# Kernel optimization log

Hardware: AMD Instinct MI355X
Metric: run time of the kernel (lower is better)

The kernel has to match this reference:

```python
import jax, jax.numpy as jnp
import numpy as np

NEG = -1e9
EPS = 1e-5


def _layernorm(x, g, b):
    m = x.mean(-1, keepdims=True)
    v = ((x - m) ** 2).mean(-1, keepdims=True)
    return (x - m) / jnp.sqrt(v + EPS) * g + b


def _layer(h_aug, H_inc, mask_neg, W1, W1_hat, ctx1, W2, W2_hat, W3, g, b):
    # h_aug: (T, H), H_inc/mask_neg: (T, E)
    H = h_aug.shape[-1]
    scale = 1.0 / jnp.sqrt(jnp.asarray(H, h_aug.dtype))
    # Stage 1: node -> hyperedge attention
    proj_hat = h_aug @ W1_hat.T                       # (T, H)
    raw = (proj_hat * ctx1).sum(-1) * scale           # (T,)
    score = raw[:, None] + mask_neg                   # (T, E)
    alpha = jax.nn.softmax(score, axis=0) * H_inc     # (T, E)
    hyper = alpha.T @ (h_aug @ W1.T)                  # (E, H)
    # Stage 2: hyperedge -> node attention
    proj2_hat = hyper @ W2_hat.T                      # (E, H)
    score_ne = (h_aug @ W3.T) @ proj2_hat.T * scale + mask_neg  # (T, E)
    beta = jax.nn.softmax(score_ne, axis=1) * H_inc   # (T, E)
    out = beta @ (hyper @ W2.T)                       # (T, H)
    return _layernorm(out + h_aug, g, b)


def reference(node_emb, H_inc, membership, W1, W1_hat, ctx1, W2, W2_hat, W3, ln_g, ln_b, region_init):
    B, N, H = node_emb.shape
    R = region_init.shape[0]
    L = W1.shape[0]
    mask_neg = jnp.where(H_inc == 0, NEG, 0.0).astype(node_emb.dtype)
    counts = jax.ops.segment_sum(jnp.ones((N,), node_emb.dtype), membership, num_segments=R)
    safe_counts = jnp.maximum(counts, 1.0)

    def per_sample(h):  # h: (N, H)
        sums = jax.ops.segment_sum(h, membership, num_segments=R)     # (R, H)
        reg = jnp.where(counts[:, None] > 0, sums / safe_counts[:, None], 0.0)
        reg = reg + region_init
        h_aug = jnp.concatenate([h, reg], axis=0)                     # (N+R, H)
        for l in range(L):
            h_aug = _layer(h_aug, H_inc, mask_neg, W1[l], W1_hat[l], ctx1[l],
                           W2[l], W2_hat[l], W3[l], ln_g[l], ln_b[l])
        return h_aug[:N]

    return jax.vmap(per_sample)(node_emb)


def setup_inputs() -> dict:
    key = jax.random.key(0)
    ks = jax.random.split(key, 12)
    B, N, R, E, H, L = 4, 8000, 16, 1024, 128, 2
    T = N + R
    w_std = 1.0 / np.sqrt(H)
    node_emb = jax.random.normal(ks[0], (B, N, H), dtype=jnp.float32)
    H_inc = (jax.random.uniform(ks[1], (T, E)) < 0.05).astype(jnp.float32)
    membership = jax.random.randint(ks[2], (N,), 0, R, dtype=jnp.int32)
    W1 = jax.random.normal(ks[3], (L, H, H), dtype=jnp.float32) * w_std
    W1_hat = jax.random.normal(ks[4], (L, H, H), dtype=jnp.float32) * w_std
    ctx1 = jax.random.normal(ks[5], (L, H), dtype=jnp.float32) * 0.02
    W2 = jax.random.normal(ks[6], (L, H, H), dtype=jnp.float32) * w_std
    W2_hat = jax.random.normal(ks[7], (L, H, H), dtype=jnp.float32) * w_std
    W3 = jax.random.normal(ks[8], (L, H, H), dtype=jnp.float32) * w_std
    ln_g = jnp.ones((L, H), dtype=jnp.float32)
    ln_b = jnp.zeros((L, H), dtype=jnp.float32)
    region_init = jax.random.normal(ks[9], (R, H), dtype=jnp.float32) * 0.02
    return {"node_emb": node_emb, "H_inc": H_inc, "membership": membership,
            "W1": W1, "W1_hat": W1_hat, "ctx1": ctx1, "W2": W2, "W2_hat": W2_hat,
            "W3": W3, "ln_g": ln_g, "ln_b": ln_b, "region_init": region_init}
```

## Files before the change

kernel.cpp:

```cpp
#include <hip/hip_runtime.h>

#define HD 128
#define CAPE 768
#define MAXR 16
#define NB_RS 128
#define RF_CH 16
#define KSTR 136
#define VSTR 72

typedef unsigned short u16;
typedef unsigned long long u64;
typedef __attribute__((ext_vector_type(8))) short bf16x8;
typedef __attribute__((ext_vector_type(4))) float f32x4;
typedef __attribute__((ext_vector_type(4))) unsigned u32x4;

__device__ inline float b2f(unsigned u){ return __uint_as_float(u << 16); }
__device__ inline float b2fhi(unsigned u){ return __uint_as_float(u & 0xffff0000u); }
__device__ inline u16 f2b(float x){
  unsigned u = __float_as_uint(x);
  return (u16)((u + 0x7fffu + ((u >> 16) & 1u)) >> 16);
}

__device__ inline float waveSum(float v){ for(int o=32;o;o>>=1) v += __shfl_down(v,o); return v; }
__device__ inline float waveMax(float v){ for(int o=32;o;o>>=1) v = fmaxf(v,__shfl_down(v,o)); return v; }

__device__ inline float blockSum128(float v, float* red){
  int j = threadIdx.x;
  float s = waveSum(v);
  __syncthreads();
  if ((j & 63) == 0) red[j >> 6] = s;
  __syncthreads();
  return red[0] + red[1];
}
__device__ inline float blockMax128(float v, float* red){
  int j = threadIdx.x;
  float s = waveMax(v);
  __syncthreads();
  if ((j & 63) == 0) red[j >> 6] = s;
  __syncthreads();
  return fmaxf(red[0], red[1]);
}

__global__ void k_count(const int* __restrict__ memb, int N, int* __restrict__ counts){
  __shared__ int h[64];
  int tid = threadIdx.x;
  if (tid < 64) h[tid] = 0;
  __syncthreads();
  for (int t = blockIdx.x*blockDim.x + tid; t < N; t += gridDim.x*blockDim.x)
    atomicAdd(&h[memb[t]], 1);
  __syncthreads();
  if (tid < 64){ int v = h[tid]; if (v) atomicAdd(&counts[tid], v); }
}

__global__ __launch_bounds__(128) void k_regsum_fast(const float* __restrict__ node,
                        const int* __restrict__ memb, int N, int R,
                        float* __restrict__ partials){
  int b = blockIdx.y, j = threadIdx.x, blk = blockIdx.x;
  int nb = gridDim.x;
  int per = (N + nb - 1) / nb;
  int t0 = blk * per;
  int t1 = t0 + per; if (t1 > N) t1 = N;
  float acc[MAXR];
  #pragma unroll
  for (int i = 0; i < MAXR; ++i) acc[i] = 0.f;
  const float* base = node + (long)b*N*HD + j;
  #pragma unroll 4
  for (int t = t0; t < t1; ++t){
    float v = base[(long)t*HD];
    int r = memb[t];
    #pragma unroll
    for (int i = 0; i < MAXR; ++i) acc[i] += (i == r) ? v : 0.f;
  }
  float* dst = partials + ((long)(b*nb + blk)*R)*HD + j;
  #pragma unroll
  for (int i = 0; i < MAXR; ++i)
    if (i < R) dst[(long)i*HD] = acc[i];
}

__global__ void k_regsum_lds(const float* __restrict__ node, const int* __restrict__ memb,
                             int N, int R, float* __restrict__ partials, int nb){
  extern __shared__ float acc[];
  int b = blockIdx.y, j = threadIdx.x;
  for (int r = 0; r < R; ++r) acc[r*HD + j] = 0.f;
  int per = (N + gridDim.x - 1) / gridDim.x;
  int t0 = blockIdx.x * per;
  int t1 = t0 + per; if (t1 > N) t1 = N;
  for (int t = t0; t < t1; ++t){
    int r = memb[t];
    acc[r*HD + j] += node[((long)b*N + t)*HD + j];
  }
  for (int r = 0; r < R; ++r)
    atomicAdd(&partials[((long)(b*nb)*R + r)*HD + j], acc[r*HD + j]);
}

__global__ __launch_bounds__(128) void k_regfin1b(const float* __restrict__ partials,
                         int nb, int redN, int R, int total, float* __restrict__ red2){
  int c = blockIdx.y;
  int i = blockIdx.x*128 + threadIdx.x;
  if (i >= total) return;
  int j = i % HD;
  int r = (i / HD) % R;
  int b = i / (HD * R);
  int per = (redN + RF_CH - 1) / RF_CH;
  int k0 = c*per, k1 = k0 + per; if (k1 > redN) k1 = redN;
  float s = 0.f;
  for (int blk = k0; blk < k1; ++blk)
    s += partials[((long)(b*nb + blk)*R + r)*HD + j];
  red2[(long)c*total + i] = s;
}

__global__ void k_regfin2(const float* __restrict__ red2, int total,
                          const int* __restrict__ counts,
                          const float* __restrict__ rinit, float* __restrict__ h_aug,
                          int N, int R, int T, int B){
  int i = blockIdx.x*blockDim.x + threadIdx.x;
  if (i >= total) return;
  int j = i % HD; int r = (i/HD) % R; int b = i/(HD*R);
  float s = 0.f;
  #pragma unroll
  for (int c = 0; c < RF_CH; ++c)
    s += red2[(long)c*total + i];
  int cnt = counts[r];
  float v = (cnt > 0) ? s / (float)cnt : 0.f;
  v += rinit[r*HD + j];
  h_aug[((long)b*T + N + r)*HD + j] = v;
}

__global__ __launch_bounds__(128) void k_copyraw(const float* __restrict__ node,
                      const float* __restrict__ v, float* __restrict__ h_aug,
                      float* __restrict__ raw, int N, int T, float scale){
  int t = blockIdx.x, b = blockIdx.y, j = threadIdx.x;
  __shared__ float red[2];
  long rowb = (long)b*T + t;
  float x;
  if (t < N){ x = node[((long)b*N + t)*HD + j]; h_aug[rowb*HD + j] = x; }
  else      { x = h_aug[rowb*HD + j]; }
  float s = blockSum128(x * v[j], red);
  if (j == 0) raw[rowb] = s * scale;
}

__global__ __launch_bounds__(256) void k_maskbuild(const float* __restrict__ Hinc, int E, int MW,
                        u64* __restrict__ maskw){
  int t = blockIdx.x;
  int wv = threadIdx.x >> 6, lane = threadIdx.x & 63;
  const float* hrow = Hinc + (long)t*E;
  for (int w = wv; w < MW; w += 4){
    int e = w*64 + lane;
    bool f = (e < E) && (hrow[e] != 0.f);
    u64 mk = __ballot(f);
    if (lane == 0) maskw[(long)t*MW + w] = mk;
  }
}

__global__ __launch_bounds__(256) void k_colbuild2(const u64* __restrict__ maskw, int T, int MW,
                           u16* __restrict__ colidx, int* __restrict__ colcnt){
  int e = blockIdx.x;
  int w = e >> 6, bit = e & 63;
  int j = threadIdx.x;
  int lane = j & 63, wv = j >> 6;
  __shared__ int wsum[4];
  int c = 0;
  for (int base = 0; base < T; base += 256){
    int t = base + j;
    bool f = (t < T) && ((maskw[(long)t*MW + w] >> bit) & 1ull);
    u64 mk = __ballot(f);
    if (lane == 0) wsum[wv] = __popcll(mk);
    __syncthreads();
    int pre = 0;
    #pragma unroll
    for (int k = 0; k < 4; ++k) pre += (k < wv) ? wsum[k] : 0;
    int tot = wsum[0] + wsum[1] + wsum[2] + wsum[3];
    if (f){
      int pos = c + pre + (int)__popcll(mk & ((1ull << lane) - 1ull));
      if (pos < CAPE) colidx[(long)e*CAPE + pos] = (u16)t;
    }
    c += tot;
    __syncthreads();
  }
  if (j == 0) colcnt[e] = (c < CAPE) ? c : CAPE;
}

__global__ void k_ctxv(const float* __restrict__ ctx1, const float* __restrict__ W1h,
                       float* __restrict__ v){
  int l = blockIdx.x, k = threadIdx.x;
  float a = 0.f;
  for (int j = 0; j < HD; ++j) a += ctx1[l*HD + j] * W1h[((long)l*HD + j)*HD + k];
  v[l*HD + k] = a;
}

__global__ void k_mm128(const float* __restrict__ W2h, const float* __restrict__ W3,
                        float* __restrict__ MqT){
  int n = blockIdx.x, l = blockIdx.y, k = threadIdx.x;
  const float* A = W2h + (long)l*HD*HD;
  const float* Bm = W3 + (long)l*HD*HD;
  float s = 0.f;
  for (int j = 0; j < HD; ++j) s += A[(long)j*HD + n] * Bm[(long)j*HD + k];
  MqT[((long)l*HD + n)*HD + k] = s;
}

__global__ __launch_bounds__(256) void k_gemmM(const float* __restrict__ A,
                       const float* __restrict__ Wa, const float* __restrict__ Wb,
                       u16* __restrict__ Ca, u16* __restrict__ Cb, int M){
  const float* W = blockIdx.y ? Wb : Wa;
  u16* C = blockIdx.y ? Cb : Ca;
  __shared__ __align__(16) u16 Ws[128][KSTR];
  __shared__ __align__(16) u16 As[64][KSTR];
  int tid = threadIdx.x;
  int row0 = blockIdx.x * 64;
  for (int i = tid; i < 128*128; i += 256){
    int r = i >> 7, c = i & 127;
    Ws[r][c] = f2b(W[(long)r*HD + c]);
  }
  for (int i = tid; i < 64*128; i += 256){
    int r = i >> 7, c = i & 127;
    int gr = row0 + r;
    As[r][c] = (gr < M) ? f2b(A[(long)gr*HD + c]) : (u16)0;
  }
  __syncthreads();

  int wave = tid >> 6, lane = tid & 63;
  int wr0 = wave * 16;
  int frow = lane & 15;
  int koff = (lane >> 4) * 8;
  f32x4 acc[8];
  #pragma unroll
  for (int f = 0; f < 8; ++f) acc[f] = (f32x4){0.f,0.f,0.f,0.f};

  #pragma unroll
  for (int ks = 0; ks < 4; ++ks){
    int kc = ks*32 + koff;
    bf16x8 av = *(const bf16x8*)&As[wr0 + frow][kc];
    #pragma unroll
    for (int f = 0; f < 8; ++f){
      bf16x8 bv = *(const bf16x8*)&Ws[f*16 + frow][kc];
      acc[f] = __builtin_amdgcn_mfma_f32_16x16x32_bf16(av, bv, acc[f], 0, 0, 0);
    }
  }

  int orow = wr0 + (lane >> 4) * 4;
  #pragma unroll
  for (int f = 0; f < 8; ++f){
    int col = f*16 + frow;
    #pragma unroll
    for (int i = 0; i < 4; ++i){
      int gr = row0 + orow + i;
      if (gr < M) C[(long)gr*HD + col] = f2b(acc[f][i]);
    }
  }
}

__global__ __launch_bounds__(256) void k_gemmW2T(const float* __restrict__ W2,
                       const u16* __restrict__ hyb, u16* __restrict__ hw2t, int E){
  int b = blockIdx.y;
  int e0 = blockIdx.x * 64;
  __shared__ __align__(16) u16 As[128][KSTR];
  __shared__ __align__(16) u16 Bs[64][KSTR];
  int tid = threadIdx.x;
  for (int i = tid; i < 128*128; i += 256){
    int r = i >> 7, c = i & 127;
    As[r][c] = f2b(W2[(long)r*HD + c]);
  }
  {
    int er = tid >> 2, q = (tid & 3)*32;
    if (e0 + er < E){
      const uint4* src = (const uint4*)(hyb + ((long)b*E + e0 + er)*HD + q);
      uint4 w0 = src[0], w1 = src[1], w2 = src[2], w3 = src[3];
      *(uint4*)&Bs[er][q]    = w0;
      *(uint4*)&Bs[er][q+8]  = w1;
      *(uint4*)&Bs[er][q+16] = w2;
      *(uint4*)&Bs[er][q+24] = w3;
    } else {
      uint4 z = {0,0,0,0};
      *(uint4*)&Bs[er][q] = z; *(uint4*)&Bs[er][q+8] = z;
      *(uint4*)&Bs[er][q+16] = z; *(uint4*)&Bs[er][q+24] = z;
    }
  }
  __syncthreads();
  int wv = tid >> 6, lane = tid & 63;
  int lc = lane & 15, lg = lane >> 4;
  f32x4 acc[2][4];
  #pragma unroll
  for (int mt=0;mt<2;++mt)
    #pragma unroll
    for (int nf=0;nf<4;++nf) acc[mt][nf] = (f32x4){0.f,0.f,0.f,0.f};
  #pragma unroll
  for (int mt=0;mt<2;++mt){
    int hr = wv*32 + mt*16 + lc;
    #pragma unroll
    for (int ks=0;ks<4;++ks){
      bf16x8 av = *(const bf16x8*)&As[hr][ks*32 + lg*8];
      #pragma unroll
      for (int nf=0;nf<4;++nf){
        bf16x8 bv = *(const bf16x8*)&Bs[nf*16+lc][ks*32 + lg*8];
        acc[mt][nf] = __builtin_amdgcn_mfma_f32_16x16x32_bf16(av, bv, acc[mt][nf], 0,0,0);
      }
    }
  }
  #pragma unroll
  for (int mt=0;mt<2;++mt){
    #pragma unroll
    for (int nf=0;nf<4;++nf){
      #pragma unroll
      for (int i=0;i<4;++i){
        int h = wv*32 + mt*16 + lg*4 + i;
        int e = e0 + nf*16 + lc;
        if (e < E) hw2t[((long)b*HD + h)*E + e] = f2b(acc[mt][nf][i]);
      }
    }
  }
}

__global__ __launch_bounds__(128) void k_edge(int swz, const float* __restrict__ raw,
                      const u16* __restrict__ proj1b,
                      const int* __restrict__ colcnt, const u16* __restrict__ colidx,
                      u16* __restrict__ hyb, int T, int E){
  int bi = blockIdx.x;
  int b, e;
  if (swz){ int x = bi & 7; b = x >> 1; e = ((bi >> 3) << 1) | (x & 1); }
  else    { b = bi / E; e = bi - b*E; }
  int j = threadIdx.x;
  int lane = j & 63, w = j >> 6;
  __shared__ float red[2];
  __shared__ float wls[CAPE];
  __shared__ int   tls[CAPE];
  __shared__ float part[128];
  int c = colcnt[e]; if (c > CAPE) c = CAPE;
  const u16* ci = colidx + (long)e*CAPE;
  const float* rawb = raw + (long)b*T;
  unsigned* orow = (unsigned*)(hyb + ((long)b*E + e)*HD);
  if (c <= 0){ if (w == 0) orow[lane] = 0u; return; }
  float lm = -1e30f;
  for (int i = j; i < c; i += 128){
    int t = ci[i];
    float v = rawb[t];
    tls[i] = t;
    wls[i] = v;
    lm = fmaxf(lm, v);
  }
  float m = blockMax128(lm, red);
  float lz = 0.f;
  for (int i = j; i < c; i += 128){
    float x = __expf(wls[i] - m);
    wls[i] = x;
    lz += x;
  }
  float Z = blockSum128(lz, red);
  float invZ = 1.f / Z;
  const u16* pb = proj1b + (long)b*T*HD + 2*lane;
  float a00=0.f,a01=0.f,a10=0.f,a11=0.f;
  int i = w;
  for (; i + 2 < c; i += 4){
    int t0v = tls[i], t1v = tls[i+2];
    float w0 = wls[i], w1 = wls[i+2];
    unsigned u0 = *(const unsigned*)(pb + (long)t0v*HD);
    unsigned u1 = *(const unsigned*)(pb + (long)t1v*HD);
    a00 += w0 * b2f(u0 & 0xffffu);  a01 += w0 * b2fhi(u0);
    a10 += w1 * b2f(u1 & 0xffffu);  a11 += w1 * b2fhi(u1);
  }
  for (; i < c; i += 2){
    float w0 = wls[i];
    unsigned u0 = *(const unsigned*)(pb + (long)tls[i]*HD);
    a00 += w0 * b2f(u0 & 0xffffu);  a01 += w0 * b2fhi(u0);
  }
  float o0 = a00 + a10, o1 = a01 + a11;
  __syncthreads();
  if (w == 1){ part[lane*2] = o0; part[lane*2+1] = o1; }
  __syncthreads();
  if (w == 0){
    o0 = (o0 + part[lane*2])   * invZ;
    o1 = (o1 + part[lane*2+1]) * invZ;
    orow[lane] = (unsigned)f2b(o0) | ((unsigned)f2b(o1) << 16);
  }
}

__global__ __launch_bounds__(256) void k_flashp(
      const u16* __restrict__ qtb, const u16* __restrict__ hyb, const u16* __restrict__ hw2t,
      const u64* __restrict__ maskw,
      u16* __restrict__ Opart, float* __restrict__ mpart, float* __restrict__ lpart,
      int T, int E, int half, float scale){
  int b = blockIdx.y, Bc = gridDim.y;
  int s = blockIdx.z, nsplit = gridDim.z;
  int t0 = blockIdx.x * 64;
  int tid = threadIdx.x;
  int wv = tid >> 6, lane = tid & 63;
  int lc = lane & 15, lg = lane >> 4;

  __shared__ __align__(16) u16 Ks[64][KSTR];
  __shared__ __align__(16) u16 Vs[128][VSTR];

  int MW = (E + 63) >> 6;
  int ntile = (E + 63) / 64;
  int et0 = s * half;
  int etend = (s == nsplit-1) ? ntile : ((s+1)*half < ntile ? (s+1)*half : ntile);

  int qrow = t0 + wv*16 + lc;
  bf16x8 qf[4];
  if (qrow < T){
    const u16* qr = qtb + ((long)b*T + qrow)*HD + lg*8;
    #pragma unroll
    for (int ks = 0; ks < 4; ++ks) qf[ks] = *(const bf16x8*)(qr + ks*32);
  } else {
    #pragma unroll
    for (int ks = 0; ks < 4; ++ks) qf[ks] = (bf16x8){0,0,0,0,0,0,0,0};
  }

  float m_s = -1e30f, l_s = 0.f;
  f32x4 Oa[8];
  #pragma unroll
  for (int f=0;f<8;++f) Oa[f] = (f32x4){0.f,0.f,0.f,0.f};

  const u16* hyB = hyb + (long)b*E*HD;
  const u16* vtB = hw2t + (long)b*HD*E;

  int kr = tid >> 2, kq = (tid & 3)*32;
  int vh = tid >> 1, vo = (tid & 1)*32;

  uint4 kreg0, kreg1, kreg2, kreg3, vreg0, vreg1, vreg2, vreg3;
  const uint4 zz = make_uint4(0u,0u,0u,0u);

  if (et0 < etend){
    int e0 = et0*64;
    if (e0 + kr < E){
      const uint4* sp = (const uint4*)(hyB + (long)(e0+kr)*HD + kq);
      kreg0=sp[0]; kreg1=sp[1]; kreg2=sp[2]; kreg3=sp[3];
    } else { kreg0=zz; kreg1=zz; kreg2=zz; kreg3=zz; }
    if (e0 + vo + 31 < E){
      const uint4* sp = (const uint4*)(vtB + (long)vh*E + e0 + vo);
      vreg0=sp[0]; vreg1=sp[1]; vreg2=sp[2]; vreg3=sp[3];
    } else {
      union { uint4 v[4]; u16 s[32]; } u;
      #pragma unroll
      for (int k=0;k<32;++k){ int e=e0+vo+k; u.s[k] = (e<E)? vtB[(long)vh*E+e] : (u16)0; }
      vreg0=u.v[0]; vreg1=u.v[1]; vreg2=u.v[2]; vreg3=u.v[3];
    }
  }

  for (int et = et0; et < etend; ++et){
    *(uint4*)&Ks[kr][kq]    = kreg0;
    *(uint4*)&Ks[kr][kq+8]  = kreg1;
    *(uint4*)&Ks[kr][kq+16] = kreg2;
    *(uint4*)&Ks[kr][kq+24] = kreg3;
    {
      int eb0 = vo;        int ne0 = eb0>>4; int ka0 = (ne0>>1)*32 + ((eb0>>2)&3)*8 + (ne0&1)*4;
      int eb1 = vo + 8;    int ne1 = eb1>>4; int ka1 = (ne1>>1)*32 + ((eb1>>2)&3)*8 + (ne1&1)*4;
      int eb2 = vo + 16;   int ne2 = eb2>>4; int ka2 = (ne2>>1)*32 + ((eb2>>2)&3)*8 + (ne2&1)*4;
      int eb3 = vo + 24;   int ne3 = eb3>>4; int ka3 = (ne3>>1)*32 + ((eb3>>2)&3)*8 + (ne3&1)*4;
      *(uint2*)&Vs[vh][ka0]   = make_uint2(vreg0.x, vreg0.y);
      *(uint2*)&Vs[vh][ka0+8] = make_uint2(vreg0.z, vreg0.w);
      *(uint2*)&Vs[vh][ka1]   = make_uint2(vreg1.x, vreg1.y);
      *(uint2*)&Vs[vh][ka1+8] = make_uint2(vreg1.z, vreg1.w);
      *(uint2*)&Vs[vh][ka2]   = make_uint2(vreg2.x, vreg2.y);
      *(uint2*)&Vs[vh][ka2+8] = make_uint2(vreg2.z, vreg2.w);
      *(uint2*)&Vs[vh][ka3]   = make_uint2(vreg3.x, vreg3.y);
      *(uint2*)&Vs[vh][ka3+8] = make_uint2(vreg3.z, vreg3.w);
    }
    __syncthreads();
    if (et + 1 < etend){
      int e0 = (et+1)*64;
      if (e0 + kr < E){
        const uint4* sp = (const uint4*)(hyB + (long)(e0+kr)*HD + kq);
        kreg0=sp[0]; kreg1=sp[1]; kreg2=sp[2]; kreg3=sp[3];
      } else { kreg0=zz; kreg1=zz; kreg2=zz; kreg3=zz; }
      if (e0 + vo + 31 < E){
        const uint4* sp = (const uint4*)(vtB + (long)vh*E + e0 + vo);
        vreg0=sp[0]; vreg1=sp[1]; vreg2=sp[2]; vreg3=sp[3];
      } else {
        union { uint4 v[4]; u16 s[32]; } u;
        #pragma unroll
        for (int k=0;k<32;++k){ int e=e0+vo+k; u.s[k] = (e<E)? vtB[(long)vh*E+e] : (u16)0; }
        vreg0=u.v[0]; vreg1=u.v[1]; vreg2=u.v[2]; vreg3=u.v[3];
      }
    }

    u64 mw = (qrow < T) ? maskw[(long)qrow*MW + et] : 0ull;

    f32x4 accS[4];
    #pragma unroll
    for (int ne=0;ne<4;++ne) accS[ne] = (f32x4){0.f,0.f,0.f,0.f};
    __builtin_amdgcn_s_setprio(1);
    #pragma unroll
    for (int ks=0;ks<4;++ks){
      #pragma unroll
      for (int ne=0;ne<4;++ne){
        bf16x8 kv = *(const bf16x8*)&Ks[ne*16+lc][ks*32 + lg*8];
        accS[ne] = __builtin_amdgcn_mfma_f32_16x16x32_bf16(kv, qf[ks], accS[ne], 0,0,0);
      }
    }
    __builtin_amdgcn_s_setprio(0);

    unsigned lo = (unsigned)mw, hi = (unsigned)(mw >> 32);
    unsigned nib[4];
    nib[0] = (lo >> (lg*4)) & 0xFu;
    nib[1] = (lo >> (16 + lg*4)) & 0xFu;
    nib[2] = (hi >> (lg*4)) & 0xFu;
    nib[3] = (hi >> (16 + lg*4)) & 0xFu;

    float p[4][4];
    float mx = -3e30f;
    #pragma unroll
    for (int ne=0;ne<4;++ne){
      #pragma unroll
      for (int r=0;r<4;++r){
        float sv = ((nib[ne] >> r) & 1u) ? accS[ne][r]*scale : -3e30f;
        p[ne][r] = sv;
        mx = fmaxf(mx, sv);
      }
    }
    mx = fmaxf(mx, __shfl_xor(mx, 16));
    mx = fmaxf(mx, __shfl_xor(mx, 32));

    float corr = 1.f;
    if (!__all(mx <= m_s + 8.f)){
      float mn = fmaxf(m_s, mx);
      corr = __expf(m_s - mn);
      m_s = mn;
      float corrO[4];
      #pragma unroll
      for (int i=0;i<4;++i) corrO[i] = __shfl(corr, lg*4 + i, 16);
      #pragma unroll
      for (int f=0;f<8;++f){
        #pragma unroll
        for (int i=0;i<4;++i) Oa[f][i] *= corrO[i];
      }
    }

    float ls = 0.f;
    #pragma unroll
    for (int ne=0;ne<4;++ne){
      #pragma unroll
      for (int r=0;r<4;++r){
        float pv = __expf(p[ne][r] - m_s);
        p[ne][r] = pv;
        ls += pv;
      }
    }
    ls += __shfl_xor(ls, 16);
    ls += __shfl_xor(ls, 32);
    l_s = l_s*corr + ls;

    unsigned pk00, pk01, pk10, pk11, pk20, pk21, pk30, pk31;
    asm("v_cvt_pk_bf16_f32 %0, %1, %2" : "=v"(pk00) : "v"(p[0][0]), "v"(p[0][1]));
    asm("v_cvt_pk_bf16_f32 %0, %1, %2" : "=v"(pk01) : "v"(p[0][2]), "v"(p[0][3]));
    asm("v_cvt_pk_bf16_f32 %0, %1, %2" : "=v"(pk10) : "v"(p[1][0]), "v"(p[1][1]));
    asm("v_cvt_pk_bf16_f32 %0, %1, %2" : "=v"(pk11) : "v"(p[1][2]), "v"(p[1][3]));
    asm("v_cvt_pk_bf16_f32 %0, %1, %2" : "=v"(pk20) : "v"(p[2][0]), "v"(p[2][1]));
    asm("v_cvt_pk_bf16_f32 %0, %1, %2" : "=v"(pk21) : "v"(p[2][2]), "v"(p[2][3]));
    asm("v_cvt_pk_bf16_f32 %0, %1, %2" : "=v"(pk30) : "v"(p[3][0]), "v"(p[3][1]));
    asm("v_cvt_pk_bf16_f32 %0, %1, %2" : "=v"(pk31) : "v"(p[3][2]), "v"(p[3][3]));

    __builtin_amdgcn_s_setprio(1);
    {
      u32x4 w0v = { pk00, pk01, pk10, pk11 };
      bf16x8 pa0 = __builtin_bit_cast(bf16x8, w0v);
      #pragma unroll
      for (int f=0;f<8;++f){
        bf16x8 vb = *(const bf16x8*)&Vs[f*16+lc][lg*8];
        Oa[f] = __builtin_amdgcn_mfma_f32_16x16x32_bf16(pa0, vb, Oa[f], 0,0,0);
      }
      u32x4 w1v = { pk20, pk21, pk30, pk31 };
      bf16x8 pa1 = __builtin_bit_cast(bf16x8, w1v);
      #pragma unroll
      for (int f=0;f<8;++f){
        bf16x8 vb = *(const bf16x8*)&Vs[f*16+lc][32 + lg*8];
        Oa[f] = __builtin_amdgcn_mfma_f32_16x16x32_bf16(pa1, vb, Oa[f], 0,0,0);
      }
    }
    __builtin_amdgcn_s_setprio(0);
    __syncthreads();
  }

  u16* Ob = Opart + (((long)s*Bc + b)*T)*HD;
  #pragma unroll
  for (int i=0;i<4;++i){
    int t = t0 + wv*16 + lg*4 + i;
    if (t >= T) continue;
    #pragma unroll
    for (int f=0;f<8;++f)
      Ob[(long)t*HD + f*16 + lc] = f2b(Oa[f][i]);
  }
  if (lg == 0 && qrow < T){
    long mlrow = ((long)s*Bc + b)*T + qrow;
    mpart[mlrow] = m_s;
    lpart[mlrow] = l_s;
  }
}

__global__ __launch_bounds__(128) void k_merge(
      const u16* __restrict__ Opart, const float* __restrict__ mpart, const float* __restrict__ lpart,
      int nsplit,
      const float* __restrict__ lng, const float* __restrict__ lnb,
      const float* __restrict__ vnext, float* __restrict__ rawnext, int writeRaw,
      float* __restrict__ h_aug, float* __restrict__ out,
      int T, int N, int writeOut, float scale){
  int t = blockIdx.x, b = blockIdx.y, j = threadIdx.x;
  int Bc = gridDim.y;
  __shared__ float red[2];
  long r0 = ((long)b)*T + t;
  long r1 = ((long)Bc + b)*T + t;
  float m0 = mpart[r0], l0 = lpart[r0];
  float m1 = (nsplit > 1) ? mpart[r1] : -1e30f;
  float l1 = (nsplit > 1) ? lpart[r1] : 0.f;
  float M = fmaxf(m0, m1);
  float c0 = __expf(m0 - M), c1 = __expf(m1 - M);
  float l = l0*c0 + l1*c1;
  float inv = (l > 0.f) ? 1.f/l : 0.f;
  float o = b2f(Opart[r0*HD + j]) * c0;
  if (nsplit > 1) o += b2f(Opart[r1*HD + j]) * c1;
  o *= inv;
  long rowb = (long)b*T + t;
  float x = o + h_aug[rowb*HD + j];
  float mean = blockSum128(x, red) * (1.f/HD);
  float d = x - mean;
  float var = blockSum128(d*d, red) * (1.f/HD);
  float y = d * rsqrtf(var + 1e-5f) * lng[j] + lnb[j];
  if (writeOut){
    if (t < N) out[((long)b*N + t)*HD + j] = y;
  } else {
    h_aug[rowb*HD + j] = y;
  }
  if (writeRaw){
    float s = blockSum128(y * vnext[j], red);
    if (j == 0) rawnext[rowb] = s * scale;
  }
}

extern "C" void kernel_launch(void* const* d_in, const int* in_sizes, int n_in,
                              void* d_out, int out_size, void* d_ws, size_t ws_size,
                              hipStream_t stream) {
  const float* node_emb = (const float*)d_in[0];
  const float* Hinc     = (const float*)d_in[1];
  const int*   memb     = (const int*)d_in[2];
  const float* W1       = (const float*)d_in[3];
  const float* W1h      = (const float*)d_in[4];
  const float* ctx1     = (const float*)d_in[5];
  const float* W2       = (const float*)d_in[6];
  const float* W2h      = (const float*)d_in[7];
  const float* W3       = (const float*)d_in[8];
  const float* lng      = (const float*)d_in[9];
  const float* lnb      = (const float*)d_in[10];
  const float* rinit    = (const float*)d_in[11];
  float* out = (float*)d_out;

  const int N  = in_sizes[2];
  const int Hd = in_sizes[3] / in_sizes[5];
  const int L  = in_sizes[5] / Hd;
  const int R  = in_sizes[11] / Hd;
  const int B  = in_sizes[0] / (N * Hd);
  const int T  = N + R;
  const int E  = in_sizes[1] / T;
  const int MW = (E + 63) / 64;
  const float scale = 1.0f / sqrtf((float)Hd);

  char* p = (char*)d_ws;
  auto carve = [&](size_t bytes){ char* r = p; p += (bytes + 255) & ~(size_t)255; return (void*)r; };
  float* h_aug  = (float*)carve((size_t)B*T*Hd*4);
  u16*   proj1b = (u16*)  carve((size_t)B*T*Hd*2);
  u16*   qtb    = (u16*)  carve((size_t)B*T*Hd*2);
  u16*   hyb    = (u16*)  carve((size_t)B*E*Hd*2);
  u16*   hw2t   = (u16*)  carve((size_t)B*Hd*E*2);
  float* MqT    = (float*)carve((size_t)L*Hd*Hd*4);
  float* rawb   = (float*)carve((size_t)B*T*4);
  float* vbuf   = (float*)carve((size_t)L*Hd*4);
  u64*   maskw  = (u64*)  carve((size_t)T*MW*8);
  int* counts   = (int*)carve((size_t)R*4);
  int* col_cnt  = (int*)carve((size_t)E*4);
  u16* col_idx  = (u16*)carve((size_t)E*CAPE*2);
  float* mpart  = (float*)carve((size_t)2*B*T*4);
  float* lpart  = (float*)carve((size_t)2*B*T*4);
  float* red2   = (float*)carve((size_t)RF_CH*B*MAXR*Hd*4);

  size_t used = (size_t)(p - (char*)d_ws);
  size_t rem  = (ws_size > used) ? (ws_size - used) : 0;
  size_t needP  = (size_t)B*NB_RS*R*Hd*4;
  size_t needO2 = (size_t)2*B*T*Hd*2;
  size_t need2 = needP > needO2 ? needP : needO2;
  int SPLIT = (rem >= need2) ? 2 : 1;
  float* partials = (float*)p;
  u16*   Opart    = (u16*)p;

  hipMemsetAsync(counts, 0, (size_t)R*4, stream);

  k_count<<<32, 256, 0, stream>>>(memb, N, counts);

  int total = B*R*Hd;
  int redN;
  if (R <= MAXR){
    k_regsum_fast<<<dim3(NB_RS, B), 128, 0, stream>>>(node_emb, memb, N, R, partials);
    redN = NB_RS;
  } else {
    hipMemsetAsync(partials, 0, (size_t)B*R*Hd*4, stream);
    k_regsum_lds<<<dim3(16, B), Hd, (size_t)R*Hd*4, stream>>>(node_emb, memb, N, R, partials, NB_RS);
    redN = 1;
  }
  k_regfin1b<<<dim3((total+127)/128, RF_CH), 128, 0, stream>>>(partials, NB_RS, redN, R, total, red2);
  k_regfin2<<<(total+255)/256, 256, 0, stream>>>(red2, total, counts, rinit, h_aug, N, R, T, B);

  k_maskbuild<<<T, 256, 0, stream>>>(Hinc, E, MW, maskw);
  k_colbuild2<<<E, 256, 0, stream>>>(maskw, T, MW, col_idx, col_cnt);

  k_ctxv<<<L, Hd, 0, stream>>>(ctx1, W1h, vbuf);
  k_mm128<<<dim3(Hd, L), Hd, 0, stream>>>(W2h, W3, MqT);
  k_copyraw<<<dim3(T, B), 128, 0, stream>>>(node_emb, vbuf, h_aug, rawb, N, T, scale);

  int MT = B*T;
  int gTm = (MT + 63)/64;
  int gTf = (T + 63)/64;
  int gEt = (E + 63)/64;
  int ntile = (E + 63)/64;
  int half = (ntile + SPLIT - 1)/SPLIT;
  int swzE = (B == 4 && (E & 1) == 0) ? 1 : 0;
  for (int l = 0; l < L; ++l){
    size_t wo = (size_t)l*Hd*Hd;
    k_gemmM<<<dim3(gTm, 2), 256, 0, stream>>>(h_aug, W1 + wo, MqT + wo, proj1b, qtb, MT);
    k_edge<<<B*E, 128, 0, stream>>>(swzE, rawb, proj1b, col_cnt, col_idx, hyb, T, E);
    k_gemmW2T<<<dim3(gEt, B), 256, 0, stream>>>(W2 + wo, hyb, hw2t, E);
    k_flashp<<<dim3(gTf, B, SPLIT), 256, 0, stream>>>(qtb, hyb, hw2t, maskw,
                                    Opart, mpart, lpart, T, E, half, scale);
    int writeRaw = (l < L-1) ? 1 : 0;
    const float* vnext = vbuf + (size_t)((l+1 < L) ? (l+1) : l)*Hd;
    k_merge<<<dim3(T, B), 128, 0, stream>>>(Opart, mpart, lpart, SPLIT,
                                    lng + wo/Hd, lnb + wo/Hd,
                                    vnext, rawb, writeRaw,
                                    h_aug, out, T, N, (l == L-1) ? 1 : 0, scale);
  }
}
```

Measured before the change: 385.3 us.

## Process two 64-row query tiles per flash block to reuse K/V tiles

Each k_flashp block now handles 128 query rows instead of 64, with every wave keeping two independent sets of Q fragments, online-softmax state and output accumulators. Each K/V tile staged in LDS now feeds twice as many MFMAs, which halves global and LDS loads per query row and interleaves two independent MFMA chains. In exchange register pressure roughly doubles for accumulators, which may lower occupancy or spill, and the grid has half as many blocks (about 63 per batch and split).

```diff
diff --git a/kernel.cpp b/kernel.cpp
--- a/kernel.cpp
+++ b/kernel.cpp
@@ -380,7 +380,7 @@
       int T, int E, int half, float scale){
   int b = blockIdx.y, Bc = gridDim.y;
   int s = blockIdx.z, nsplit = gridDim.z;
-  int t0 = blockIdx.x * 64;
+  int t0 = blockIdx.x * 128;
   int tid = threadIdx.x;
   int wv = tid >> 6, lane = tid & 63;
   int lc = lane & 15, lg = lane >> 4;
@@ -393,21 +393,30 @@
   int et0 = s * half;
   int etend = (s == nsplit-1) ? ntile : ((s+1)*half < ntile ? (s+1)*half : ntile);
 
-  int qrow = t0 + wv*16 + lc;
-  bf16x8 qf[4];
-  if (qrow < T){
-    const u16* qr = qtb + ((long)b*T + qrow)*HD + lg*8;
-    #pragma unroll
-    for (int ks = 0; ks < 4; ++ks) qf[ks] = *(const bf16x8*)(qr + ks*32);
+  int qrowA = t0 + wv*16 + lc;
+  int qrowB = qrowA + 64;
+  bf16x8 qfA[4], qfB[4];
+  if (qrowA < T){
+    const u16* qr = qtb + ((long)b*T + qrowA)*HD + lg*8;
+    #pragma unroll
+    for (int ks = 0; ks < 4; ++ks) qfA[ks] = *(const bf16x8*)(qr + ks*32);
   } else {
     #pragma unroll
-    for (int ks = 0; ks < 4; ++ks) qf[ks] = (bf16x8){0,0,0,0,0,0,0,0};
-  }
-
-  float m_s = -1e30f, l_s = 0.f;
-  f32x4 Oa[8];
-  #pragma unroll
-  for (int f=0;f<8;++f) Oa[f] = (f32x4){0.f,0.f,0.f,0.f};
+    for (int ks = 0; ks < 4; ++ks) qfA[ks] = (bf16x8){0,0,0,0,0,0,0,0};
+  }
+  if (qrowB < T){
+    const u16* qr = qtb + ((long)b*T + qrowB)*HD + lg*8;
+    #pragma unroll
+    for (int ks = 0; ks < 4; ++ks) qfB[ks] = *(const bf16x8*)(qr + ks*32);
+  } else {
+    #pragma unroll
+    for (int ks = 0; ks < 4; ++ks) qfB[ks] = (bf16x8){0,0,0,0,0,0,0,0};
+  }
+
+  float m_A = -1e30f, l_A = 0.f, m_B = -1e30f, l_B = 0.f;
+  f32x4 OaA[8], OaB[8];
+  #pragma unroll
+  for (int f=0;f<8;++f){ OaA[f] = (f32x4){0.f,0.f,0.f,0.f}; OaB[f] = (f32x4){0.f,0.f,0.f,0.f}; }
 
   const u16* hyB = hyb + (long)b*E*HD;
   const u16* vtB = hw2t + (long)b*HD*E;
@@ -472,97 +481,131 @@
       }
     }
 
-    u64 mw = (qrow < T) ? maskw[(long)qrow*MW + et] : 0ull;
-
-    f32x4 accS[4];
-    #pragma unroll
-    for (int ne=0;ne<4;++ne) accS[ne] = (f32x4){0.f,0.f,0.f,0.f};
+    u64 mwA = (qrowA < T) ? maskw[(long)qrowA*MW + et] : 0ull;
+    u64 mwB = (qrowB < T) ? maskw[(long)qrowB*MW + et] : 0ull;
+
+    f32x4 accSA[4], accSB[4];
+    #pragma unroll
+    for (int ne=0;ne<4;++ne){ accSA[ne] = (f32x4){0.f,0.f,0.f,0.f}; accSB[ne] = (f32x4){0.f,0.f,0.f,0.f}; }
     __builtin_amdgcn_s_setprio(1);
     #pragma unroll
     for (int ks=0;ks<4;++ks){
       #pragma unroll
       for (int ne=0;ne<4;++ne){
         bf16x8 kv = *(const bf16x8*)&Ks[ne*16+lc][ks*32 + lg*8];
-        accS[ne] = __builtin_amdgcn_mfma_f32_16x16x32_bf16(kv, qf[ks], accS[ne], 0,0,0);
+        accSA[ne] = __builtin_amdgcn_mfma_f32_16x16x32_bf16(kv, qfA[ks], accSA[ne], 0,0,0);
+        accSB[ne] = __builtin_amdgcn_mfma_f32_16x16x32_bf16(kv, qfB[ks], accSB[ne], 0,0,0);
       }
     }
     __builtin_amdgcn_s_setprio(0);
 
-    unsigned lo = (unsigned)mw, hi = (unsigned)(mw >> 32);
-    unsigned nib[4];
-    nib[0] = (lo >> (lg*4)) & 0xFu;
-    nib[1] = (lo >> (16 + lg*4)) & 0xFu;
-    nib[2] = (hi >> (lg*4)) & 0xFu;
-    nib[3] = (hi >> (16 + lg*4)) & 0xFu;
-
-    float p[4][4];
-    float mx = -3e30f;
+    unsigned loA = (unsigned)mwA, hiA = (unsigned)(mwA >> 32);
+    unsigned loB = (unsigned)mwB, hiB = (unsigned)(mwB >> 32);
+    unsigned nibA[4], nibB[4];
+    nibA[0] = (loA >> (lg*4)) & 0xFu;  nibA[1] = (loA >> (16 + lg*4)) & 0xFu;
+    nibA[2] = (hiA >> (lg*4)) & 0xFu;  nibA[3] = (hiA >> (16 + lg*4)) & 0xFu;
+    nibB[0] = (loB >> (lg*4)) & 0xFu;  nibB[1] = (loB >> (16 + lg*4)) & 0xFu;
+    nibB[2] = (hiB >> (lg*4)) & 0xFu;  nibB[3] = (hiB >> (16 + lg*4)) & 0xFu;
+
+    float pA[4][4], pB[4][4];
+    float mxA = -3e30f, mxB = -3e30f;
     #pragma unroll
     for (int ne=0;ne<4;++ne){
       #pragma unroll
       for (int r=0;r<4;++r){
-        float sv = ((nib[ne] >> r) & 1u) ? accS[ne][r]*scale : -3e30f;
-        p[ne][r] = sv;
-        mx = fmaxf(mx, sv);
-      }
-    }
-    mx = fmaxf(mx, __shfl_xor(mx, 16));
-    mx = fmaxf(mx, __shfl_xor(mx, 32));
-
-    float corr = 1.f;
-    if (!__all(mx <= m_s + 8.f)){
-      float mn = fmaxf(m_s, mx);
-      corr = __expf(m_s - mn);
-      m_s = mn;
-      float corrO[4];
-      #pragma unroll
-      for (int i=0;i<4;++i) corrO[i] = __shfl(corr, lg*4 + i, 16);
+        float svA = ((nibA[ne] >> r) & 1u) ? accSA[ne][r]*scale : -3e30f;
+        float svB = ((nibB[ne] >> r) & 1u) ? accSB[ne][r]*scale : -3e30f;
+        pA[ne][r] = svA; pB[ne][r] = svB;
+        mxA = fmaxf(mxA, svA); mxB = fmaxf(mxB, svB);
+      }
+    }
+    mxA = fmaxf(mxA, __shfl_xor(mxA, 16)); mxA = fmaxf(mxA, __shfl_xor(mxA, 32));
+    mxB = fmaxf(mxB, __shfl_xor(mxB, 16)); mxB = fmaxf(mxB, __shfl_xor(mxB, 32));
+
+    float corrA = 1.f;
+    if (!__all(mxA <= m_A + 8.f)){
+      float mn = fmaxf(m_A, mxA);
+      corrA = __expf(m_A - mn);
+      m_A = mn;
+      float cO[4];
+      #pragma unroll
+      for (int i=0;i<4;++i) cO[i] = __shfl(corrA, lg*4 + i, 16);
       #pragma unroll
       for (int f=0;f<8;++f){
         #pragma unroll
-        for (int i=0;i<4;++i) Oa[f][i] *= corrO[i];
-      }
-    }
-
-    float ls = 0.f;
+        for (int i=0;i<4;++i) OaA[f][i] *= cO[i];
+      }
+    }
+    float corrB = 1.f;
+    if (!__all(mxB <= m_B + 8.f)){
+      float mn = fmaxf(m_B, mxB);
+      corrB = __expf(m_B - mn);
+      m_B = mn;
+      float cO[4];
+      #pragma unroll
+      for (int i=0;i<4;++i) cO[i] = __shfl(corrB, lg*4 + i, 16);
+      #pragma unroll
+      for (int f=0;f<8;++f){
+        #pragma unroll
+        for (int i=0;i<4;++i) OaB[f][i] *= cO[i];
+      }
+    }
+
+    float lsA = 0.f, lsB = 0.f;
     #pragma unroll
     for (int ne=0;ne<4;++ne){
       #pragma unroll
       for (int r=0;r<4;++r){
-        float pv = __expf(p[ne][r] - m_s);
-        p[ne][r] = pv;
-        ls += pv;
-      }
-    }
-    ls += __shfl_xor(ls, 16);
-    ls += __shfl_xor(ls, 32);
-    l_s = l_s*corr + ls;
-
-    unsigned pk00, pk01, pk10, pk11, pk20, pk21, pk30, pk31;
-    asm("v_cvt_pk_bf16_f32 %0, %1, %2" : "=v"(pk00) : "v"(p[0][0]), "v"(p[0][1]));
-    asm("v_cvt_pk_bf16_f32 %0, %1, %2" : "=v"(pk01) : "v"(p[0][2]), "v"(p[0][3]));
-    asm("v_cvt_pk_bf16_f32 %0, %1, %2" : "=v"(pk10) : "v"(p[1][0]), "v"(p[1][1]));
-    asm("v_cvt_pk_bf16_f32 %0, %1, %2" : "=v"(pk11) : "v"(p[1][2]), "v"(p[1][3]));
-    asm("v_cvt_pk_bf16_f32 %0, %1, %2" : "=v"(pk20) : "v"(p[2][0]), "v"(p[2][1]));
-    asm("v_cvt_pk_bf16_f32 %0, %1, %2" : "=v"(pk21) : "v"(p[2][2]), "v"(p[2][3]));
-    asm("v_cvt_pk_bf16_f32 %0, %1, %2" : "=v"(pk30) : "v"(p[3][0]), "v"(p[3][1]));
-    asm("v_cvt_pk_bf16_f32 %0, %1, %2" : "=v"(pk31) : "v"(p[3][2]), "v"(p[3][3]));
+        float pvA = __expf(pA[ne][r] - m_A);
+        float pvB = __expf(pB[ne][r] - m_B);
+        pA[ne][r] = pvA; pB[ne][r] = pvB;
+        lsA += pvA; lsB += pvB;
+      }
+    }
+    lsA += __shfl_xor(lsA, 16); lsA += __shfl_xor(lsA, 32);
+    lsB += __shfl_xor(lsB, 16); lsB += __shfl_xor(lsB, 32);
+    l_A = l_A*corrA + lsA;
+    l_B = l_B*corrB + lsB;
+
+    unsigned pkA[8], pkB[8];
+    asm("v_cvt_pk_bf16_f32 %0, %1, %2" : "=v"(pkA[0]) : "v"(pA[0][0]), "v"(pA[0][1]));
+    asm("v_cvt_pk_bf16_f32 %0, %1, %2" : "=v"(pkA[1]) : "v"(pA[0][2]), "v"(pA[0][3]));
+    asm("v_cvt_pk_bf16_f32 %0, %1, %2" : "=v"(pkA[2]) : "v"(pA[1][0]), "v"(pA[1][1]));
+    asm("v_cvt_pk_bf16_f32 %0, %1, %2" : "=v"(pkA[3]) : "v"(pA[1][2]), "v"(pA[1][3]));
+    asm("v_cvt_pk_bf16_f32 %0, %1, %2" : "=v"(pkA[4]) : "v"(pA[2][0]), "v"(pA[2][1]));
+    asm("v_cvt_pk_bf16_f32 %0, %1, %2" : "=v"(pkA[5]) : "v"(pA[2][2]), "v"(pA[2][3]));
+    asm("v_cvt_pk_bf16_f32 %0, %1, %2" : "=v"(pkA[6]) : "v"(pA[3][0]), "v"(pA[3][1]));
+    asm("v_cvt_pk_bf16_f32 %0, %1, %2" : "=v"(pkA[7]) : "v"(pA[3][2]), "v"(pA[3][3]));
+    asm("v_cvt_pk_bf16_f32 %0, %1, %2" : "=v"(pkB[0]) : "v"(pB[0][0]), "v"(pB[0][1]));
+    asm("v_cvt_pk_bf16_f32 %0, %1, %2" : "=v"(pkB[1]) : "v"(pB[0][2]), "v"(pB[0][3]));
+    asm("v_cvt_pk_bf16_f32 %0, %1, %2" : "=v"(pkB[2]) : "v"(pB[1][0]), "v"(pB[1][1]));
+    asm("v_cvt_pk_bf16_f32 %0, %1, %2" : "=v"(pkB[3]) : "v"(pB[1][2]), "v"(pB[1][3]));
+    asm("v_cvt_pk_bf16_f32 %0, %1, %2" : "=v"(pkB[4]) : "v"(pB[2][0]), "v"(pB[2][1]));
+    asm("v_cvt_pk_bf16_f32 %0, %1, %2" : "=v"(pkB[5]) : "v"(pB[2][2]), "v"(pB[2][3]));
+    asm("v_cvt_pk_bf16_f32 %0, %1, %2" : "=v"(pkB[6]) : "v"(pB[3][0]), "v"(pB[3][1]));
+    asm("v_cvt_pk_bf16_f32 %0, %1, %2" : "=v"(pkB[7]) : "v"(pB[3][2]), "v"(pB[3][3]));
 
     __builtin_amdgcn_s_setprio(1);
     {
-      u32x4 w0v = { pk00, pk01, pk10, pk11 };
-      bf16x8 pa0 = __builtin_bit_cast(bf16x8, w0v);
+      u32x4 wA0 = { pkA[0], pkA[1], pkA[2], pkA[3] };
+      u32x4 wB0 = { pkB[0], pkB[1], pkB[2], pkB[3] };
+      bf16x8 paA0 = __builtin_bit_cast(bf16x8, wA0);
+      bf16x8 paB0 = __builtin_bit_cast(bf16x8, wB0);
       #pragma unroll
       for (int f=0;f<8;++f){
         bf16x8 vb = *(const bf16x8*)&Vs[f*16+lc][lg*8];
-        Oa[f] = __builtin_amdgcn_mfma_f32_16x16x32_bf16(pa0, vb, Oa[f], 0,0,0);
-      }
-      u32x4 w1v = { pk20, pk21, pk30, pk31 };
-      bf16x8 pa1 = __builtin_bit_cast(bf16x8, w1v);
+        OaA[f] = __builtin_amdgcn_mfma_f32_16x16x32_bf16(paA0, vb, OaA[f], 0,0,0);
+        OaB[f] = __builtin_amdgcn_mfma_f32_16x16x32_bf16(paB0, vb, OaB[f], 0,0,0);
+      }
+      u32x4 wA1 = { pkA[4], pkA[5], pkA[6], pkA[7] };
+      u32x4 wB1 = { pkB[4], pkB[5], pkB[6], pkB[7] };
+      bf16x8 paA1 = __builtin_bit_cast(bf16x8, wA1);
+      bf16x8 paB1 = __builtin_bit_cast(bf16x8, wB1);
       #pragma unroll
       for (int f=0;f<8;++f){
         bf16x8 vb = *(const bf16x8*)&Vs[f*16+lc][32 + lg*8];
-        Oa[f] = __builtin_amdgcn_mfma_f32_16x16x32_bf16(pa1, vb, Oa[f], 0,0,0);
+        OaA[f] = __builtin_amdgcn_mfma_f32_16x16x32_bf16(paA1, vb, OaA[f], 0,0,0);
+        OaB[f] = __builtin_amdgcn_mfma_f32_16x16x32_bf16(paB1, vb, OaB[f], 0,0,0);
       }
     }
     __builtin_amdgcn_s_setprio(0);
@@ -572,16 +615,30 @@
   u16* Ob = Opart + (((long)s*Bc + b)*T)*HD;
   #pragma unroll
   for (int i=0;i<4;++i){
-    int t = t0 + wv*16 + lg*4 + i;
-    if (t >= T) continue;
-    #pragma unroll
-    for (int f=0;f<8;++f)
-      Ob[(long)t*HD + f*16 + lc] = f2b(Oa[f][i]);
-  }
-  if (lg == 0 && qrow < T){
-    long mlrow = ((long)s*Bc + b)*T + qrow;
-    mpart[mlrow] = m_s;
-    lpart[mlrow] = l_s;
+    int tA = t0 + wv*16 + lg*4 + i;
+    if (tA < T){
+      #pragma unroll
+      for (int f=0;f<8;++f)
+        Ob[(long)tA*HD + f*16 + lc] = f2b(OaA[f][i]);
+    }
+    int tB = tA + 64;
+    if (tB < T){
+      #pragma unroll
+      for (int f=0;f<8;++f)
+        Ob[(long)tB*HD + f*16 + lc] = f2b(OaB[f][i]);
+    }
+  }
+  if (lg == 0){
+    if (qrowA < T){
+      long mlrow = ((long)s*Bc + b)*T + qrowA;
+      mpart[mlrow] = m_A;
+      lpart[mlrow] = l_A;
+    }
+    if (qrowB < T){
+      long mlrow = ((long)s*Bc + b)*T + qrowB;
+      mpart[mlrow] = m_B;
+      lpart[mlrow] = l_B;
+    }
   }
 }
 
@@ -704,7 +761,7 @@
 
   int MT = B*T;
   int gTm = (MT + 63)/64;
-  int gTf = (T + 63)/64;
+  int gTf = (T + 127)/128;
   int gEt = (E + 63)/64;
   int ntile = (E + 63)/64;
   int half = (ntile + SPLIT - 1)/SPLIT;
```

Result: slower. 397.6 us (+3.2%).
